# Optimization experiments

Hardware: AMD Instinct MI355X
Metric: run time of the kernel (lower is better)

The kernel has to match this reference:

```python
import math
import jax, jax.numpy as jnp
import numpy as np

N, D = 16384, 1024


def setup_inputs() -> dict:
    key = jax.random.key(0)
    k1, k2 = jax.random.split(key)
    return {
        "image_embeddings_aligned": jax.random.normal(k1, (N, D), dtype=jnp.float32),
        "text_embeddings_aligned": jax.random.normal(k2, (N, D), dtype=jnp.float32),
        "logit_scale": jnp.asarray(math.log(20.0), dtype=jnp.float32),  # stored as log(init)
        "logit_bias": jnp.asarray(-10.0, dtype=jnp.float32),
    }


def _l2_normalize(x, eps=1e-12):
    # matches F.normalize(p=2, dim=-1)
    n = jnp.linalg.norm(x, axis=-1, keepdims=True)
    return x / jnp.maximum(n, eps)


def reference(image_embeddings_aligned, text_embeddings_aligned, logit_scale, logit_bias):
    img = _l2_normalize(image_embeddings_aligned)
    txt = _l2_normalize(text_embeddings_aligned)
    # [N, N] pairwise logits
    logits = jnp.exp(logit_scale) * jnp.einsum("nd,md->nm", img, txt) + logit_bias
    n = logits.shape[0]
    labels = 2.0 * jnp.eye(n, dtype=logits.dtype) - 1.0  # +1 on diagonal, -1 off
    loss_matrix = jax.nn.log_sigmoid(labels * logits)
    siglip_loss = -jnp.mean(loss_matrix)  # total_loss (structure_lambda == 0)
    return siglip_loss
```

## Files before the change

kernel.cpp:

```cpp
#include <hip/hip_runtime.h>

#define NROWS 16384
#define DIM   1024
#define QSCALE 32.0f
#define E8M0S  0x7A7A7A7Au

typedef int    v4i    __attribute__((ext_vector_type(4)));
typedef int    v8i    __attribute__((ext_vector_type(8)));
typedef float  f32x16 __attribute__((ext_vector_type(16)));

__device__ __forceinline__ void glds16(const void* g, void* l) {
    __builtin_amdgcn_global_load_lds(
        (const __attribute__((address_space(1))) void*)g,
        (__attribute__((address_space(3))) void*)l,
        16, 0, 0);
}

__device__ __forceinline__ float fexp2(float x) {
#if __has_builtin(__builtin_amdgcn_exp2f)
    return __builtin_amdgcn_exp2f(x);
#else
    return exp2f(x);
#endif
}
__device__ __forceinline__ float flog2(float x) {
#if __has_builtin(__builtin_amdgcn_logf)
    return __builtin_amdgcn_logf(x);
#else
    return log2f(x);
#endif
}

__device__ __forceinline__ unsigned fp4_nib(float y) {
    unsigned s = (__float_as_uint(y) >> 31) << 3;
    float a = fminf(fabsf(y), 6.0f);
    unsigned c = (unsigned)(a >= 0.25f) + (unsigned)(a >= 0.75f) +
                 (unsigned)(a >= 1.25f) + (unsigned)(a >= 1.75f) +
                 (unsigned)(a >= 2.5f)  + (unsigned)(a >= 3.5f)  +
                 (unsigned)(a >= 5.0f);
    return c | s;
}

__global__ __launch_bounds__(256) void norm_fused(
    const float* __restrict__ img,
    const float* __restrict__ txt,
    unsigned char* __restrict__ imgQ,
    unsigned char* __restrict__ txtQ,
    const float* __restrict__ lscale,
    const float* __restrict__ lbias,
    float* __restrict__ diagPart) {
    const int t    = threadIdx.x;
    const int lane = t & 63;
    const int wave = t >> 6;
    const int gw   = blockIdx.x * 4 + wave;
    const float sc   = __expf(lscale[0]);
    const float bias = lbias[0];

    for (int row = gw; row < NROWS; row += 8192) {
        const float4* pi = (const float4*)(img + (size_t)row * DIM);
        const float4* pt = (const float4*)(txt + (size_t)row * DIM);
        float4 vi[4], vt[4];
        float ssi = 0.0f, sst = 0.0f, dot = 0.0f;
        #pragma unroll
        for (int j = 0; j < 4; ++j) {
            vi[j] = pi[lane + 64 * j];
            vt[j] = pt[lane + 64 * j];
            ssi += vi[j].x*vi[j].x + vi[j].y*vi[j].y + vi[j].z*vi[j].z + vi[j].w*vi[j].w;
            sst += vt[j].x*vt[j].x + vt[j].y*vt[j].y + vt[j].z*vt[j].z + vt[j].w*vt[j].w;
            dot += vi[j].x*vt[j].x + vi[j].y*vt[j].y + vi[j].z*vt[j].z + vi[j].w*vt[j].w;
        }
        #pragma unroll
        for (int off = 1; off < 64; off <<= 1) {
            ssi += __shfl_xor(ssi, off, 64);
            sst += __shfl_xor(sst, off, 64);
            dot += __shfl_xor(dot, off, 64);
        }
        const float ii = 1.0f / fmaxf(sqrtf(ssi), 1e-12f);
        const float it = 1.0f / fmaxf(sqrtf(sst), 1e-12f);
        if (lane == 0) diagPart[row] = -fmaf(sc, dot * ii * it, bias);

        const float qi = ii * QSCALE, qt = it * QSCALE;
        ushort* oi = (ushort*)(imgQ + (size_t)row * 512);
        ushort* ot = (ushort*)(txtQ + (size_t)row * 512);
        #pragma unroll
        for (int j = 0; j < 4; ++j) {
            unsigned p = fp4_nib(vi[j].x * qi)        | (fp4_nib(vi[j].y * qi) << 4) |
                         (fp4_nib(vi[j].z * qi) << 8) | (fp4_nib(vi[j].w * qi) << 12);
            unsigned q = fp4_nib(vt[j].x * qt)        | (fp4_nib(vt[j].y * qt) << 4) |
                         (fp4_nib(vt[j].z * qt) << 8) | (fp4_nib(vt[j].w * qt) << 12);
            oi[lane + 64 * j] = (ushort)p;
            ot[lane + 64 * j] = (ushort)q;
        }
    }
}

__global__ __launch_bounds__(256, 1) void siglip_gemm(
    const unsigned char* __restrict__ A,
    const unsigned char* __restrict__ B,
    const float* __restrict__ lscale,
    const float* __restrict__ lbias,
    float* __restrict__ gemmPart)
{
    __shared__ unsigned char sA[2][256 * 128];
    __shared__ unsigned char sB[2][128 * 128];
    __shared__ float wred[4];

    const int t    = threadIdx.x;
    const int lane = t & 63;
    const int wave = t >> 6;
    const int wr   = wave >> 1;
    const int wc   = wave & 1;
    const int r31  = lane & 31;
    const int h    = lane >> 5;
    const int xr   = (r31 & 7) ^ ((r31 >> 4) & 1);

    const int GRID_N = NROWS / 128;
    const int GM = 16;
    int b = blockIdx.x;
    int group = b / (GM * GRID_N);
    int ing   = b % (GM * GRID_N);
    int brow  = group * GM + (ing % GM);
    int bcol  = ing / GM;

    const size_t aBase = (size_t)brow * 256;
    const size_t bBase = (size_t)bcol * 128;

    const int srow = lane >> 3;
    const int c0   = (lane & 7) ^ srow;
    const int d01  = (c0 & 1) ? -16 : 16;

    const unsigned char* aP = A + (size_t)(aBase + wave * 64 + srow) * 512 + c0 * 16;
    const unsigned char* bP = B + (size_t)(bBase + wave * 32 + srow) * 512 + c0 * 16;

    int rbA[4], rbB[2];
    #pragma unroll
    for (int i = 0; i < 4; ++i) rbA[i] = (wr * 128 + i * 32 + r31) * 128;
    #pragma unroll
    for (int i = 0; i < 2; ++i) rbB[i] = (wc * 64 + i * 32 + r31) * 128;

    f32x16 acc[4][2] = {};

    {
        char* la = ((char*)sA[0]) + wave * 8192;
        char* lb = ((char*)sB[0]) + wave * 4096;
        #pragma unroll
        for (int j = 0; j < 8; ++j) {
            const int tog = ((j >> 1) & 1) ? d01 : 0;
            glds16(aP + j * 8 * 512 + tog, la + j * 1024);
        }
        #pragma unroll
        for (int j = 0; j < 4; ++j) {
            const int tog = ((j >> 1) & 1) ? d01 : 0;
            glds16(bP + j * 8 * 512 + tog, lb + j * 1024);
        }
    }
    __syncthreads();

    #pragma unroll
    for (int k = 0; k < 4; ++k) {
        const int cur = k & 1;

        if (k < 3) {
            const unsigned char* aN = aP + (k + 1) * 128;
            const unsigned char* bN = bP + (k + 1) * 128;
            char* la = ((char*)sA[cur ^ 1]) + wave * 8192;
            char* lb = ((char*)sB[cur ^ 1]) + wave * 4096;
            #pragma unroll
            for (int j = 0; j < 8; ++j) {
                const int tog = ((j >> 1) & 1) ? d01 : 0;
                glds16(aN + j * 8 * 512 + tog, la + j * 1024);
            }
            #pragma unroll
            for (int j = 0; j < 4; ++j) {
                const int tog = ((j >> 1) & 1) ? d01 : 0;
                glds16(bN + j * 8 * 512 + tog, lb + j * 1024);
            }
        }

        #pragma unroll
        for (int ks = 0; ks < 4; ++ks) {
            const int s = ((ks * 2 + h) ^ xr) * 16;
            v8i af[4], bf[2];
            #pragma unroll
            for (int i = 0; i < 4; ++i) {
                v4i v = *(const v4i*)(sA[cur] + rbA[i] + s);
                af[i] = __builtin_shufflevector(v, v, 0, 1, 2, 3, -1, -1, -1, -1);
            }
            #pragma unroll
            for (int i = 0; i < 2; ++i) {
                v4i v = *(const v4i*)(sB[cur] + rbB[i] + s);
                bf[i] = __builtin_shufflevector(v, v, 0, 1, 2, 3, -1, -1, -1, -1);
            }
            #pragma unroll
            for (int mi = 0; mi < 4; ++mi)
                #pragma unroll
                for (int ni = 0; ni < 2; ++ni)
                    acc[mi][ni] = __builtin_amdgcn_mfma_scale_f32_32x32x64_f8f6f4(
                        af[mi], bf[ni], acc[mi][ni],
                        4, 4,
                        0, (int)E8M0S,
                        0, (int)E8M0S);
        }

        __syncthreads();
    }

    const float l2e   = 1.44269504088896341f;
    const float scale = __expf(lscale[0]);
    const float aCo   = scale * l2e;
    const float bCo   = lbias[0] * l2e;
    float local = 0.0f;
    #pragma unroll
    for (int mi = 0; mi < 4; ++mi)
        #pragma unroll
        for (int ni = 0; ni < 2; ++ni)
            #pragma unroll
            for (int r = 0; r < 16; r += 4) {
                float e0 = fexp2(fmaf(aCo, acc[mi][ni][r + 0], bCo));
                float e1 = fexp2(fmaf(aCo, acc[mi][ni][r + 1], bCo));
                float e2 = fexp2(fmaf(aCo, acc[mi][ni][r + 2], bCo));
                float e3 = fexp2(fmaf(aCo, acc[mi][ni][r + 3], bCo));
                float p  = ((1.0f + e0) * (1.0f + e1)) *
                           ((1.0f + e2) * (1.0f + e3));
                local += flog2(p);
            }

    #pragma unroll
    for (int off = 32; off > 0; off >>= 1) local += __shfl_down(local, off, 64);
    if (lane == 0) wred[wave] = local;
    __syncthreads();
    if (t == 0)
        gemmPart[blockIdx.x] =
            (wred[0] + wred[1] + wred[2] + wred[3]) * 0.69314718055994531f;
}

__global__ __launch_bounds__(1024) void finalize_kernel(
    const float* __restrict__ parts, float* __restrict__ out) {
    __shared__ float wr[16];
    const int t    = threadIdx.x;
    const int lane = t & 63;
    const int wave = t >> 6;
    const float4* p4 = (const float4*)parts;
    float s = 0.0f;
    for (int i = t; i < 6144; i += 1024) {
        float4 v = p4[i];
        s += v.x + v.y + v.z + v.w;
    }
    #pragma unroll
    for (int off = 32; off > 0; off >>= 1) s += __shfl_down(s, off, 64);
    if (lane == 0) wr[wave] = s;
    __syncthreads();
    if (t == 0) {
        float tot = 0.0f;
        #pragma unroll
        for (int i = 0; i < 16; ++i) tot += wr[i];
        out[0] = tot / 268435456.0f;
    }
}

extern "C" void kernel_launch(void* const* d_in, const int* in_sizes, int n_in,
                              void* d_out, int out_size, void* d_ws, size_t ws_size,
                              hipStream_t stream) {
    const float* img    = (const float*)d_in[0];
    const float* txt    = (const float*)d_in[1];
    const float* lscale = (const float*)d_in[2];
    const float* lbias  = (const float*)d_in[3];
    float* out = (float*)d_out;

    char* ws = (char*)d_ws;
    unsigned char* imgQ = (unsigned char*)ws;
    unsigned char* txtQ = (unsigned char*)(ws + (size_t)NROWS * 512);
    float* parts   = (float*)(ws + (size_t)2 * NROWS * 512);
    float* diagPart = parts;
    float* gemmPart = parts + NROWS;

    norm_fused<<<2048, 256, 0, stream>>>(img, txt, imgQ, txtQ, lscale, lbias, diagPart);
    siglip_gemm<<<dim3((NROWS / 256) * (NROWS / 128)), 256, 0, stream>>>(
        imgQ, txtQ, lscale, lbias, gemmPart);
    finalize_kernel<<<1, 1024, 0, stream>>>(parts, out);
}
```

Before: 376.0 us.

## Enlarge GEMM tile to 256x256 with 8 waves and hoist LDS fragment loads

The GEMM block tile grows from 256x128 to 256x256, run by 8 waves in a 2x4 layout. This halves the number of blocks and cuts global/L2 traffic per output element. All LDS fragment reads for the current k-slice are hoisted ahead of issuing the next async global-to-LDS prefetch, which lets LDS reads overlap with the MFMA chain. The cost is 128KB of LDS per block, which likely limits occupancy to one block per CU despite the launch bound of 2, plus higher register pressure from holding 16+8 fragments.

```diff
diff --git a/kernel.cpp b/kernel.cpp
--- a/kernel.cpp
+++ b/kernel.cpp
@@ -94,7 +94,7 @@
     }
 }
 
-__global__ __launch_bounds__(256, 1) void siglip_gemm(
+__global__ __launch_bounds__(512, 2) void siglip_gemm(
     const unsigned char* __restrict__ A,
     const unsigned char* __restrict__ B,
     const float* __restrict__ lscale,
@@ -102,19 +102,19 @@
     float* __restrict__ gemmPart)
 {
     __shared__ unsigned char sA[2][256 * 128];
-    __shared__ unsigned char sB[2][128 * 128];
-    __shared__ float wred[4];
+    __shared__ unsigned char sB[2][256 * 128];
+    __shared__ float wred[8];
 
     const int t    = threadIdx.x;
     const int lane = t & 63;
     const int wave = t >> 6;
-    const int wr   = wave >> 1;
-    const int wc   = wave & 1;
+    const int wr   = wave >> 2;
+    const int wc   = wave & 3;
     const int r31  = lane & 31;
     const int h    = lane >> 5;
     const int xr   = (r31 & 7) ^ ((r31 >> 4) & 1);
 
-    const int GRID_N = NROWS / 128;
+    const int GRID_N = NROWS / 256;
     const int GM = 16;
     int b = blockIdx.x;
     int group = b / (GM * GRID_N);
@@ -123,13 +123,13 @@
     int bcol  = ing / GM;
 
     const size_t aBase = (size_t)brow * 256;
-    const size_t bBase = (size_t)bcol * 128;
+    const size_t bBase = (size_t)bcol * 256;
 
     const int srow = lane >> 3;
     const int c0   = (lane & 7) ^ srow;
     const int d01  = (c0 & 1) ? -16 : 16;
 
-    const unsigned char* aP = A + (size_t)(aBase + wave * 64 + srow) * 512 + c0 * 16;
+    const unsigned char* aP = A + (size_t)(aBase + wave * 32 + srow) * 512 + c0 * 16;
     const unsigned char* bP = B + (size_t)(bBase + wave * 32 + srow) * 512 + c0 * 16;
 
     int rbA[4], rbB[2];
@@ -141,16 +141,12 @@
     f32x16 acc[4][2] = {};
 
     {
-        char* la = ((char*)sA[0]) + wave * 8192;
+        char* la = ((char*)sA[0]) + wave * 4096;
         char* lb = ((char*)sB[0]) + wave * 4096;
         #pragma unroll
-        for (int j = 0; j < 8; ++j) {
+        for (int j = 0; j < 4; ++j) {
             const int tog = ((j >> 1) & 1) ? d01 : 0;
             glds16(aP + j * 8 * 512 + tog, la + j * 1024);
-        }
-        #pragma unroll
-        for (int j = 0; j < 4; ++j) {
-            const int tog = ((j >> 1) & 1) ? d01 : 0;
             glds16(bP + j * 8 * 512 + tog, lb + j * 1024);
         }
     }
@@ -159,47 +155,49 @@
     #pragma unroll
     for (int k = 0; k < 4; ++k) {
         const int cur = k & 1;
+
+        v4i af[4][4], bf[4][2];
+        #pragma unroll
+        for (int ks = 0; ks < 4; ++ks) {
+            const int s = ((ks * 2 + h) ^ xr) * 16;
+            #pragma unroll
+            for (int i = 0; i < 4; ++i)
+                af[ks][i] = *(const v4i*)(sA[cur] + rbA[i] + s);
+            #pragma unroll
+            for (int n = 0; n < 2; ++n)
+                bf[ks][n] = *(const v4i*)(sB[cur] + rbB[n] + s);
+        }
 
         if (k < 3) {
             const unsigned char* aN = aP + (k + 1) * 128;
             const unsigned char* bN = bP + (k + 1) * 128;
-            char* la = ((char*)sA[cur ^ 1]) + wave * 8192;
+            char* la = ((char*)sA[cur ^ 1]) + wave * 4096;
             char* lb = ((char*)sB[cur ^ 1]) + wave * 4096;
             #pragma unroll
-            for (int j = 0; j < 8; ++j) {
+            for (int j = 0; j < 4; ++j) {
                 const int tog = ((j >> 1) & 1) ? d01 : 0;
                 glds16(aN + j * 8 * 512 + tog, la + j * 1024);
-            }
-            #pragma unroll
-            for (int j = 0; j < 4; ++j) {
-                const int tog = ((j >> 1) & 1) ? d01 : 0;
                 glds16(bN + j * 8 * 512 + tog, lb + j * 1024);
             }
         }
 
         #pragma unroll
         for (int ks = 0; ks < 4; ++ks) {
-            const int s = ((ks * 2 + h) ^ xr) * 16;
-            v8i af[4], bf[2];
-            #pragma unroll
-            for (int i = 0; i < 4; ++i) {
-                v4i v = *(const v4i*)(sA[cur] + rbA[i] + s);
-                af[i] = __builtin_shufflevector(v, v, 0, 1, 2, 3, -1, -1, -1, -1);
-            }
-            #pragma unroll
-            for (int i = 0; i < 2; ++i) {
-                v4i v = *(const v4i*)(sB[cur] + rbB[i] + s);
-                bf[i] = __builtin_shufflevector(v, v, 0, 1, 2, 3, -1, -1, -1, -1);
-            }
-            #pragma unroll
-            for (int mi = 0; mi < 4; ++mi)
+            #pragma unroll
+            for (int mi = 0; mi < 4; ++mi) {
+                v8i a8 = __builtin_shufflevector(af[ks][mi], af[ks][mi],
+                                                 0, 1, 2, 3, -1, -1, -1, -1);
                 #pragma unroll
-                for (int ni = 0; ni < 2; ++ni)
+                for (int ni = 0; ni < 2; ++ni) {
+                    v8i b8 = __builtin_shufflevector(bf[ks][ni], bf[ks][ni],
+                                                     0, 1, 2, 3, -1, -1, -1, -1);
                     acc[mi][ni] = __builtin_amdgcn_mfma_scale_f32_32x32x64_f8f6f4(
-                        af[mi], bf[ni], acc[mi][ni],
+                        a8, b8, acc[mi][ni],
                         4, 4,
                         0, (int)E8M0S,
                         0, (int)E8M0S);
+                }
+            }
         }
 
         __syncthreads();
@@ -229,9 +227,12 @@
     for (int off = 32; off > 0; off >>= 1) local += __shfl_down(local, off, 64);
     if (lane == 0) wred[wave] = local;
     __syncthreads();
-    if (t == 0)
-        gemmPart[blockIdx.x] =
-            (wred[0] + wred[1] + wred[2] + wred[3]) * 0.69314718055994531f;
+    if (t == 0) {
+        float tot = 0.0f;
+        #pragma unroll
+        for (int i = 0; i < 8; ++i) tot += wred[i];
+        gemmPart[blockIdx.x] = tot * 0.69314718055994531f;
+    }
 }
 
 __global__ __launch_bounds__(1024) void finalize_kernel(
@@ -242,7 +243,7 @@
     const int wave = t >> 6;
     const float4* p4 = (const float4*)parts;
     float s = 0.0f;
-    for (int i = t; i < 6144; i += 1024) {
+    for (int i = t; i < 5120; i += 1024) {
         float4 v = p4[i];
         s += v.x + v.y + v.z + v.w;
     }
@@ -275,7 +276,7 @@
     float* gemmPart = parts + NROWS;
 
     norm_fused<<<2048, 256, 0, stream>>>(img, txt, imgQ, txtQ, lscale, lbias, diagPart);
-    siglip_gemm<<<dim3((NROWS / 256) * (NROWS / 128)), 256, 0, stream>>>(
+    siglip_gemm<<<dim3((NROWS / 256) * (NROWS / 256)), 512, 0, stream>>>(
         imgQ, txtQ, lscale, lbias, gemmPart);
     finalize_kernel<<<1, 1024, 0, stream>>>(parts, out);
 }
```

New measurement: 312.0 us. 1.21x faster.

## Shrink GEMM tile to 128x128, single-buffer LDS, raise occupancy, XCD-aware mapping

Applied to the files above, without the earlier changes.

Reduces the per-block tile from 256x128 to 128x128 and drops LDS double buffering, so each block uses 32KB of LDS and fewer accumulator registers. Launch bounds now request 4 blocks per CU, relying on block-level concurrency rather than intra-block prefetch to hide load latency. The block-to-tile mapping is changed to group column tiles by XCD for L2 locality, and s_setprio is wrapped around the MFMA bursts. The finalize kernel now reads the larger number of partial sums. The risk is more global traffic per FLOP from smaller tiles, plus exposed load latency now that compute waits at a barrier for each K-step's loads.

```diff
diff --git a/kernel.cpp b/kernel.cpp
--- a/kernel.cpp
+++ b/kernel.cpp
@@ -94,15 +94,15 @@
     }
 }
 
-__global__ __launch_bounds__(256, 1) void siglip_gemm(
+__global__ __launch_bounds__(256, 4) void siglip_gemm(
     const unsigned char* __restrict__ A,
     const unsigned char* __restrict__ B,
     const float* __restrict__ lscale,
     const float* __restrict__ lbias,
     float* __restrict__ gemmPart)
 {
-    __shared__ unsigned char sA[2][256 * 128];
-    __shared__ unsigned char sB[2][128 * 128];
+    __shared__ unsigned char sA[128 * 128];
+    __shared__ unsigned char sB[128 * 128];
     __shared__ float wred[4];
 
     const int t    = threadIdx.x;
@@ -114,95 +114,77 @@
     const int h    = lane >> 5;
     const int xr   = (r31 & 7) ^ ((r31 >> 4) & 1);
 
-    const int GRID_N = NROWS / 128;
-    const int GM = 16;
-    int b = blockIdx.x;
-    int group = b / (GM * GRID_N);
-    int ing   = b % (GM * GRID_N);
-    int brow  = group * GM + (ing % GM);
-    int bcol  = ing / GM;
-
-    const size_t aBase = (size_t)brow * 256;
+    const int b    = blockIdx.x;
+    const int xcd  = b & 7;
+    const int lb   = b >> 3;
+    const int bcol = xcd * 16 + (lb & 15);
+    const int brow = lb >> 4;
+
+    const size_t aBase = (size_t)brow * 128;
     const size_t bBase = (size_t)bcol * 128;
 
     const int srow = lane >> 3;
     const int c0   = (lane & 7) ^ srow;
     const int d01  = (c0 & 1) ? -16 : 16;
 
-    const unsigned char* aP = A + (size_t)(aBase + wave * 64 + srow) * 512 + c0 * 16;
+    const unsigned char* aP = A + (size_t)(aBase + wave * 32 + srow) * 512 + c0 * 16;
     const unsigned char* bP = B + (size_t)(bBase + wave * 32 + srow) * 512 + c0 * 16;
-
-    int rbA[4], rbB[2];
-    #pragma unroll
-    for (int i = 0; i < 4; ++i) rbA[i] = (wr * 128 + i * 32 + r31) * 128;
+    char* la  = ((char*)sA) + wave * 4096;
+    char* lbp = ((char*)sB) + wave * 4096;
+
+    int rbA[2], rbB[2];
+    #pragma unroll
+    for (int i = 0; i < 2; ++i) rbA[i] = (wr * 64 + i * 32 + r31) * 128;
     #pragma unroll
     for (int i = 0; i < 2; ++i) rbB[i] = (wc * 64 + i * 32 + r31) * 128;
 
-    f32x16 acc[4][2] = {};
-
-    {
-        char* la = ((char*)sA[0]) + wave * 8192;
-        char* lb = ((char*)sB[0]) + wave * 4096;
-        #pragma unroll
-        for (int j = 0; j < 8; ++j) {
-            const int tog = ((j >> 1) & 1) ? d01 : 0;
-            glds16(aP + j * 8 * 512 + tog, la + j * 1024);
-        }
-        #pragma unroll
-        for (int j = 0; j < 4; ++j) {
-            const int tog = ((j >> 1) & 1) ? d01 : 0;
-            glds16(bP + j * 8 * 512 + tog, lb + j * 1024);
-        }
+    f32x16 acc[2][2] = {};
+
+    #pragma unroll
+    for (int j = 0; j < 4; ++j) {
+        const int tog = ((j >> 1) & 1) ? d01 : 0;
+        glds16(aP + j * 4096 + tog, la + j * 1024);
+        glds16(bP + j * 4096 + tog, lbp + j * 1024);
     }
     __syncthreads();
 
     #pragma unroll
     for (int k = 0; k < 4; ++k) {
-        const int cur = k & 1;
+        #pragma unroll
+        for (int ks = 0; ks < 4; ++ks) {
+            const int s = ((ks * 2 + h) ^ xr) * 16;
+            v4i a0 = *(const v4i*)(sA + rbA[0] + s);
+            v4i a1 = *(const v4i*)(sA + rbA[1] + s);
+            v4i b0 = *(const v4i*)(sB + rbB[0] + s);
+            v4i b1 = *(const v4i*)(sB + rbB[1] + s);
+            v8i A0 = __builtin_shufflevector(a0, a0, 0, 1, 2, 3, -1, -1, -1, -1);
+            v8i A1 = __builtin_shufflevector(a1, a1, 0, 1, 2, 3, -1, -1, -1, -1);
+            v8i B0 = __builtin_shufflevector(b0, b0, 0, 1, 2, 3, -1, -1, -1, -1);
+            v8i B1 = __builtin_shufflevector(b1, b1, 0, 1, 2, 3, -1, -1, -1, -1);
+            __builtin_amdgcn_s_setprio(1);
+            acc[0][0] = __builtin_amdgcn_mfma_scale_f32_32x32x64_f8f6f4(
+                A0, B0, acc[0][0], 4, 4, 0, (int)E8M0S, 0, (int)E8M0S);
+            acc[0][1] = __builtin_amdgcn_mfma_scale_f32_32x32x64_f8f6f4(
+                A0, B1, acc[0][1], 4, 4, 0, (int)E8M0S, 0, (int)E8M0S);
+            acc[1][0] = __builtin_amdgcn_mfma_scale_f32_32x32x64_f8f6f4(
+                A1, B0, acc[1][0], 4, 4, 0, (int)E8M0S, 0, (int)E8M0S);
+            acc[1][1] = __builtin_amdgcn_mfma_scale_f32_32x32x64_f8f6f4(
+                A1, B1, acc[1][1], 4, 4, 0, (int)E8M0S, 0, (int)E8M0S);
+            __builtin_amdgcn_s_setprio(0);
+        }
 
         if (k < 3) {
+            __syncthreads();
             const unsigned char* aN = aP + (k + 1) * 128;
             const unsigned char* bN = bP + (k + 1) * 128;
-            char* la = ((char*)sA[cur ^ 1]) + wave * 8192;
-            char* lb = ((char*)sB[cur ^ 1]) + wave * 4096;
-            #pragma unroll
-            for (int j = 0; j < 8; ++j) {
-                const int tog = ((j >> 1) & 1) ? d01 : 0;
-                glds16(aN + j * 8 * 512 + tog, la + j * 1024);
-            }
             #pragma unroll
             for (int j = 0; j < 4; ++j) {
                 const int tog = ((j >> 1) & 1) ? d01 : 0;
-                glds16(bN + j * 8 * 512 + tog, lb + j * 1024);
+                glds16(aN + j * 4096 + tog, la + j * 1024);
+                glds16(bN + j * 4096 + tog, lbp + j * 1024);
             }
-        }
-
-        #pragma unroll
-        for (int ks = 0; ks < 4; ++ks) {
-            const int s = ((ks * 2 + h) ^ xr) * 16;
-            v8i af[4], bf[2];
-            #pragma unroll
-            for (int i = 0; i < 4; ++i) {
-                v4i v = *(const v4i*)(sA[cur] + rbA[i] + s);
-                af[i] = __builtin_shufflevector(v, v, 0, 1, 2, 3, -1, -1, -1, -1);
-            }
-            #pragma unroll
-            for (int i = 0; i < 2; ++i) {
-                v4i v = *(const v4i*)(sB[cur] + rbB[i] + s);
-                bf[i] = __builtin_shufflevector(v, v, 0, 1, 2, 3, -1, -1, -1, -1);
-            }
-            #pragma unroll
-            for (int mi = 0; mi < 4; ++mi)
-                #pragma unroll
-                for (int ni = 0; ni < 2; ++ni)
-                    acc[mi][ni] = __builtin_amdgcn_mfma_scale_f32_32x32x64_f8f6f4(
-                        af[mi], bf[ni], acc[mi][ni],
-                        4, 4,
-                        0, (int)E8M0S,
-                        0, (int)E8M0S);
-        }
-
-        __syncthreads();
+            __syncthreads();
+        }
     }
 
     const float l2e   = 1.44269504088896341f;
@@ -211,7 +193,7 @@
     const float bCo   = lbias[0] * l2e;
     float local = 0.0f;
     #pragma unroll
-    for (int mi = 0; mi < 4; ++mi)
+    for (int mi = 0; mi < 2; ++mi)
         #pragma unroll
         for (int ni = 0; ni < 2; ++ni)
             #pragma unroll
@@ -242,7 +224,7 @@
     const int wave = t >> 6;
     const float4* p4 = (const float4*)parts;
     float s = 0.0f;
-    for (int i = t; i < 6144; i += 1024) {
+    for (int i = t; i < 8192; i += 1024) {
         float4 v = p4[i];
         s += v.x + v.y + v.z + v.w;
     }
@@ -275,7 +257,7 @@
     float* gemmPart = parts + NROWS;
 
     norm_fused<<<2048, 256, 0, stream>>>(img, txt, imgQ, txtQ, lscale, lbias, diagPart);
-    siglip_gemm<<<dim3((NROWS / 256) * (NROWS / 128)), 256, 0, stream>>>(
+    siglip_gemm<<<dim3((NROWS / 128) * (NROWS / 128)), 256, 0, stream>>>(
         imgQ, txtQ, lscale, lbias, gemmPart);
     finalize_kernel<<<1, 1024, 0, stream>>>(parts, out);
 }
```

New measurement: 310.2 us. -17.5%, faster.
